# Performance work log

Measured on AMD Instinct MI355X. Metric: run time of the kernel, lower is better.

Reference implementation:

```python
import jax, jax.numpy as jnp
import numpy as np

EMBED_DIM = 768
NUM_HEADS = 12
HEAD_DIM = EMBED_DIM // NUM_HEADS
SCALE = HEAD_DIM ** -0.5


def setup_inputs() -> dict:
    key = jax.random.key(0)
    k_x, k_qkv, k_pw, k_pb = jax.random.split(key, 4)
    B, N, C = 8, 1024, EMBED_DIM
    x = jax.random.normal(k_x, (B, N, C), dtype=jnp.float32)
    # nn.Linear(embed_dim, 3*embed_dim, bias=False): weight [3C, C]
    w_qkv = jax.random.normal(k_qkv, (3 * C, C), dtype=jnp.float32) * (C ** -0.5)
    # nn.Linear(embed_dim, embed_dim): weight [C, C], bias [C]
    w_proj = jax.random.normal(k_pw, (C, C), dtype=jnp.float32) * (C ** -0.5)
    b_proj = jax.random.normal(k_pb, (C,), dtype=jnp.float32) * 0.01
    return {"x": x, "w_qkv": w_qkv, "w_proj": w_proj, "b_proj": b_proj}


def reference(x, w_qkv, w_proj, b_proj):
    B, N, C = x.shape
    H, D = NUM_HEADS, HEAD_DIM
    # qkv projection: [B, N, 3C] -> [3, B, H, N, D]
    qkv = jnp.einsum('bnc,ec->bne', x, w_qkv)
    qkv = qkv.reshape(B, N, 3, H, D).transpose(2, 0, 3, 1, 4)
    q, k, v = qkv[0], qkv[1], qkv[2]
    # explicit attention matrix [B, H, N, N]
    attn = jax.nn.softmax(jnp.einsum('bhnd,bhmd->bhnm', q, k) * SCALE, axis=-1)
    # attn @ v -> [B, N, C]
    out = jnp.einsum('bhnm,bhmd->bhnd', attn, v)
    out = out.transpose(0, 2, 1, 3).reshape(B, N, C)
    out = jnp.einsum('bnc,oc->bno', out, w_proj) + b_proj
    return out, attn
```

## Files before the change

kernel.cpp:

```cpp
#include <hip/hip_runtime.h>

#define B_ 8
#define N_ 1024
#define C_ 768
#define H_ 12
#define D_ 64
#define SCALE_ 0.125f

typedef _Float16 v8h __attribute__((ext_vector_type(8)));
typedef float v4f __attribute__((ext_vector_type(4)));

__device__ __forceinline__ void gload_lds16(const void* g, void* l) {
    __builtin_amdgcn_global_load_lds((const __attribute__((address_space(1))) void*)g,
                                     (__attribute__((address_space(3))) void*)l, 16, 0, 0);
}

__global__ __launch_bounds__(256) void cast_f2h(const float* __restrict__ src,
                                                _Float16* __restrict__ dst, int n8) {
    const int i = blockIdx.x * 256 + threadIdx.x;
    if (i < n8) {
        const v4f a = *(const v4f*)&src[(size_t)i * 8];
        const v4f b = *(const v4f*)&src[(size_t)i * 8 + 4];
        v8h o;
        o[0] = (_Float16)a[0]; o[1] = (_Float16)a[1]; o[2] = (_Float16)a[2]; o[3] = (_Float16)a[3];
        o[4] = (_Float16)b[0]; o[5] = (_Float16)b[1]; o[6] = (_Float16)b[2]; o[7] = (_Float16)b[3];
        *(v8h*)&dst[(size_t)i * 8] = o;
    }
}

__global__ __launch_bounds__(256) void gemm_qkv(const _Float16* __restrict__ X,
                                                const _Float16* __restrict__ W,
                                                _Float16* __restrict__ qh,
                                                _Float16* __restrict__ kh,
                                                _Float16* __restrict__ vth) {
    __shared__ _Float16 As[128 * 32];
    __shared__ _Float16 Bs[128 * 32];
    const int t = threadIdx.x;
    const int w = t >> 6, l = t & 63;
    const int q4 = l >> 4, c0 = l & 15;
    const int wm = w & 1, wn = w >> 1;
    const int m0 = blockIdx.x * 128, n0 = blockIdx.y * 128;
    const int sc8 = (t & 3) * 8;
    v4f acc[4][4] = {};
    for (int k0 = 0; k0 < C_; k0 += 32) {
        #pragma unroll
        for (int i = 0; i < 2; ++i) {
            const int row = i * 64 + (t >> 2);
            gload_lds16(&X[(size_t)(m0 + row) * C_ + k0 + sc8], &As[(i * 256 + t) * 8]);
            gload_lds16(&W[(size_t)(n0 + row) * C_ + k0 + sc8], &Bs[(i * 256 + t) * 8]);
        }
        __syncthreads();
        v8h a[4], b[4];
        #pragma unroll
        for (int mi = 0; mi < 4; ++mi)
            a[mi] = *(const v8h*)&As[(wm * 64 + mi * 16 + c0) * 32 + q4 * 8];
        #pragma unroll
        for (int ni = 0; ni < 4; ++ni)
            b[ni] = *(const v8h*)&Bs[(wn * 64 + ni * 16 + c0) * 32 + q4 * 8];
        #pragma unroll
        for (int mi = 0; mi < 4; ++mi)
            #pragma unroll
            for (int ni = 0; ni < 4; ++ni)
                acc[mi][ni] = __builtin_amdgcn_mfma_f32_16x16x32_f16(a[mi], b[ni], acc[mi][ni], 0, 0, 0);
        __syncthreads();
    }
    const int which = n0 / C_;
    const int nbase = n0 % C_;
    #pragma unroll
    for (int ni = 0; ni < 4; ++ni) {
        const int n = nbase + wn * 64 + ni * 16 + c0;
        const int h = n >> 6, d = n & 63;
        #pragma unroll
        for (int mi = 0; mi < 4; ++mi) {
            #pragma unroll
            for (int r = 0; r < 4; ++r) {
                const int m = m0 + wm * 64 + mi * 16 + q4 * 4 + r;
                const int b = m >> 10, nn = m & 1023;
                const _Float16 val = (_Float16)acc[mi][ni][r];
                if (which == 0)
                    qh[((size_t)(b * H_ + h) * N_ + nn) * D_ + d] = val;
                else if (which == 1)
                    kh[((size_t)(b * H_ + h) * N_ + nn) * D_ + d] = val;
                else
                    vth[((size_t)(b * H_ + h) * D_ + d) * N_ + nn] = val;
            }
        }
    }
}

__global__ __launch_bounds__(256) void attn_fused(const _Float16* __restrict__ qh,
                                                  const _Float16* __restrict__ kh,
                                                  const _Float16* __restrict__ vth,
                                                  float* __restrict__ attn,
                                                  _Float16* __restrict__ oah) {
    __shared__ _Float16 Qs[2 * 16 * 32];
    __shared__ _Float16 Ks[2 * 128 * 32];
    __shared__ _Float16 Vt[4 * 64 * 32];
    __shared__ float Ps[16 * 132];
    __shared__ float redm[64], reds[64];
    const int t = threadIdx.x;
    const int w = t >> 6, l = t & 63;
    const int q4 = l >> 4, c0 = l & 15;
    const int mt = blockIdx.x, bh = blockIdx.y;
    const size_t qkbase = (size_t)bh * N_ * D_;
    const size_t vtbase = (size_t)bh * D_ * N_;

    if (w < 2)
        gload_lds16(&qh[qkbase + (size_t)(mt * 16 + (l >> 2)) * D_ + w * 32 + (l & 3) * 8],
                    &Qs[t * 8]);
    #pragma unroll
    for (int i = 0; i < 4; ++i) {
        const int idx = i * 256 + t;
        const int p = idx >> 9, row = (idx & 511) >> 2, c8 = (idx & 3) * 8;
        gload_lds16(&kh[qkbase + (size_t)row * D_ + p * 32 + c8], &Ks[idx * 8]);
    }
    __syncthreads();
    v8h a0 = *(const v8h*)&Qs[c0 * 32 + q4 * 8];
    v8h a1 = *(const v8h*)&Qs[512 + c0 * 32 + q4 * 8];

    v4f S[16];
    #pragma unroll
    for (int i = 0; i < 16; ++i) S[i] = (v4f){0.f, 0.f, 0.f, 0.f};

    for (int c = 0; c < 8; ++c) {
        #pragma unroll
        for (int h2 = 0; h2 < 2; ++h2) {
            const int roff = (h2 * 64 + w * 16 + c0) * 32 + q4 * 8;
            const v8h b0 = *(const v8h*)&Ks[roff];
            const v8h b1 = *(const v8h*)&Ks[4096 + roff];
            v4f acc = __builtin_amdgcn_mfma_f32_16x16x32_f16(a0, b0, S[c * 2 + h2], 0, 0, 0);
            S[c * 2 + h2] = __builtin_amdgcn_mfma_f32_16x16x32_f16(a1, b1, acc, 0, 0, 0);
        }
        if (c < 7) {
            __syncthreads();
            #pragma unroll
            for (int i = 0; i < 4; ++i) {
                const int idx = i * 256 + t;
                const int p = idx >> 9, row = (idx & 511) >> 2, c8 = (idx & 3) * 8;
                gload_lds16(&kh[qkbase + (size_t)((c + 1) * 128 + row) * D_ + p * 32 + c8],
                            &Ks[idx * 8]);
            }
            __syncthreads();
        }
    }

    float mrow[4] = {-1e30f, -1e30f, -1e30f, -1e30f};
    #pragma unroll
    for (int kt = 0; kt < 16; ++kt)
        #pragma unroll
        for (int r = 0; r < 4; ++r) mrow[r] = fmaxf(mrow[r], S[kt][r]);
    #pragma unroll
    for (int r = 0; r < 4; ++r) {
        #pragma unroll
        for (int mask = 8; mask; mask >>= 1)
            mrow[r] = fmaxf(mrow[r], __shfl_xor(mrow[r], mask, 16));
    }
    if (c0 == 0) {
        #pragma unroll
        for (int r = 0; r < 4; ++r) redm[w * 16 + q4 * 4 + r] = mrow[r];
    }
    __syncthreads();
    #pragma unroll
    for (int r = 0; r < 4; ++r) {
        float mm = redm[q4 * 4 + r];
        mm = fmaxf(mm, redm[16 + q4 * 4 + r]);
        mm = fmaxf(mm, redm[32 + q4 * 4 + r]);
        mm = fmaxf(mm, redm[48 + q4 * 4 + r]);
        mrow[r] = mm;
    }
    float srow[4] = {0.f, 0.f, 0.f, 0.f};
    #pragma unroll
    for (int kt = 0; kt < 16; ++kt)
        #pragma unroll
        for (int r = 0; r < 4; ++r) {
            const float e = __expf((S[kt][r] - mrow[r]) * SCALE_);
            S[kt][r] = e;
            srow[r] += e;
        }
    #pragma unroll
    for (int r = 0; r < 4; ++r) {
        #pragma unroll
        for (int mask = 8; mask; mask >>= 1) srow[r] += __shfl_xor(srow[r], mask, 16);
    }
    if (c0 == 0) {
        #pragma unroll
        for (int r = 0; r < 4; ++r) reds[w * 16 + q4 * 4 + r] = srow[r];
    }
    __syncthreads();
    float inv[4];
    #pragma unroll
    for (int r = 0; r < 4; ++r)
        inv[r] = 1.0f / (reds[q4 * 4 + r] + reds[16 + q4 * 4 + r] +
                         reds[32 + q4 * 4 + r] + reds[48 + q4 * 4 + r]);

    v4f O = {0.f, 0.f, 0.f, 0.f};
    for (int s = 0; s < 8; ++s) {
        #pragma unroll
        for (int kt2 = 0; kt2 < 2; ++kt2)
            #pragma unroll
            for (int r = 0; r < 4; ++r)
                Ps[(q4 * 4 + r) * 132 + kt2 * 64 + w * 16 + c0] = S[s * 2 + kt2][r] * inv[r];
        #pragma unroll
        for (int i = 0; i < 4; ++i)
            gload_lds16(&vth[vtbase + (size_t)(t >> 2) * N_ + s * 128 + i * 32 + (t & 3) * 8],
                        &Vt[(i * 256 + t) * 8]);
        __syncthreads();
        #pragma unroll
        for (int i = 0; i < 2; ++i) {
            const int cidx = i * 256 + t;
            const int row = cidx >> 5, col = (cidx & 31) * 4;
            *(v4f*)&attn[((size_t)bh * N_ + mt * 16 + row) * N_ + s * 128 + col] =
                *(const v4f*)&Ps[row * 132 + col];
        }
        #pragma unroll
        for (int kk = 0; kk < 4; ++kk) {
            const float* pp = &Ps[c0 * 132 + kk * 32 + q4 * 8];
            const v4f p0 = *(const v4f*)pp;
            const v4f p1 = *(const v4f*)(pp + 4);
            v8h af;
            af[0] = (_Float16)p0[0]; af[1] = (_Float16)p0[1];
            af[2] = (_Float16)p0[2]; af[3] = (_Float16)p0[3];
            af[4] = (_Float16)p1[0]; af[5] = (_Float16)p1[1];
            af[6] = (_Float16)p1[2]; af[7] = (_Float16)p1[3];
            const v8h bf = *(const v8h*)&Vt[kk * 2048 + (w * 16 + c0) * 32 + q4 * 8];
            O = __builtin_amdgcn_mfma_f32_16x16x32_f16(af, bf, O, 0, 0, 0);
        }
        __syncthreads();
    }
    const int b = bh / H_, h = bh % H_;
    #pragma unroll
    for (int r = 0; r < 4; ++r)
        oah[((size_t)b * N_ + mt * 16 + q4 * 4 + r) * C_ + h * D_ + w * 16 + c0] = (_Float16)O[r];
}

__global__ __launch_bounds__(256) void gemm_proj(const _Float16* __restrict__ X,
                                                 const _Float16* __restrict__ W,
                                                 const float* __restrict__ Bias,
                                                 float* __restrict__ out) {
    __shared__ _Float16 As[128 * 32];
    __shared__ _Float16 Bs[128 * 32];
    const int t = threadIdx.x;
    const int w = t >> 6, l = t & 63;
    const int q4 = l >> 4, c0 = l & 15;
    const int wm = w & 1, wn = w >> 1;
    const int m0 = blockIdx.x * 128, n0 = blockIdx.y * 128;
    const int sc8 = (t & 3) * 8;
    v4f acc[4][4] = {};
    for (int k0 = 0; k0 < C_; k0 += 32) {
        #pragma unroll
        for (int i = 0; i < 2; ++i) {
            const int row = i * 64 + (t >> 2);
            gload_lds16(&X[(size_t)(m0 + row) * C_ + k0 + sc8], &As[(i * 256 + t) * 8]);
            gload_lds16(&W[(size_t)(n0 + row) * C_ + k0 + sc8], &Bs[(i * 256 + t) * 8]);
        }
        __syncthreads();
        v8h a[4], b[4];
        #pragma unroll
        for (int mi = 0; mi < 4; ++mi)
            a[mi] = *(const v8h*)&As[(wm * 64 + mi * 16 + c0) * 32 + q4 * 8];
        #pragma unroll
        for (int ni = 0; ni < 4; ++ni)
            b[ni] = *(const v8h*)&Bs[(wn * 64 + ni * 16 + c0) * 32 + q4 * 8];
        #pragma unroll
        for (int mi = 0; mi < 4; ++mi)
            #pragma unroll
            for (int ni = 0; ni < 4; ++ni)
                acc[mi][ni] = __builtin_amdgcn_mfma_f32_16x16x32_f16(a[mi], b[ni], acc[mi][ni], 0, 0, 0);
        __syncthreads();
    }
    #pragma unroll
    for (int ni = 0; ni < 4; ++ni) {
        const int n = n0 + wn * 64 + ni * 16 + c0;
        const float bias = Bias[n];
        #pragma unroll
        for (int mi = 0; mi < 4; ++mi) {
            #pragma unroll
            for (int r = 0; r < 4; ++r) {
                const int m = m0 + wm * 64 + mi * 16 + q4 * 4 + r;
                out[(size_t)m * C_ + n] = acc[mi][ni][r] + bias;
            }
        }
    }
}

extern "C" void kernel_launch(void* const* d_in, const int* in_sizes, int n_in,
                              void* d_out, int out_size, void* d_ws, size_t ws_size,
                              hipStream_t stream) {
    const float* x      = (const float*)d_in[0];
    const float* w_qkv  = (const float*)d_in[1];
    const float* w_proj = (const float*)d_in[2];
    const float* b_proj = (const float*)d_in[3];

    float* out  = (float*)d_out;
    float* attn = out + (size_t)B_ * N_ * C_;

    const size_t NX  = (size_t)B_ * N_ * C_;
    const size_t NWQ = (size_t)3 * C_ * C_;
    const size_t NWP = (size_t)C_ * C_;
    _Float16* xh  = (_Float16*)d_ws;
    _Float16* wqh = xh + NX;
    _Float16* wph = wqh + NWQ;
    _Float16* qh  = wph + NWP;
    _Float16* kh  = qh + NX;
    _Float16* vth = kh + NX;
    _Float16* oah = vth + NX;

    cast_f2h<<<dim3((int)(NX / 8 / 256)), 256, 0, stream>>>(x, xh, (int)(NX / 8));
    cast_f2h<<<dim3((int)(NWQ / 8 / 256)), 256, 0, stream>>>(w_qkv, wqh, (int)(NWQ / 8));
    cast_f2h<<<dim3((int)(NWP / 8 / 256)), 256, 0, stream>>>(w_proj, wph, (int)(NWP / 8));

    gemm_qkv  <<<dim3(64, 18), 256, 0, stream>>>(xh, wqh, qh, kh, vth);
    attn_fused<<<dim3(64, 96), 256, 0, stream>>>(qh, kh, vth, attn, oah);
    gemm_proj <<<dim3(64, 6), 256, 0, stream>>>(oah, wph, b_proj, out);
}
```

Measured before the change: 675.2 us.

## Double-buffer GEMM and attention tiles, widen attention blocks to 32 query rows

Both GEMMs now double-buffer their LDS tiles so the next K-slice loads while MFMAs run on the current one, and drop one barrier per iteration. The attention kernel is restructured to 512 threads covering 32 query rows, with double-buffered K, P and V^T tiles in 64-column chunks. The attention-matrix and output writes use nontemporal stores. This aims to hide global-load latency and reduce write-back traffic, at the cost of more LDS per block and a more complex sync schedule that could lower occupancy.

After: 577.9 us. 14.4% less time.

```diff
diff --git a/kernel.cpp b/kernel.cpp
--- a/kernel.cpp
+++ b/kernel.cpp
@@ -33,30 +33,43 @@
                                                 _Float16* __restrict__ qh,
                                                 _Float16* __restrict__ kh,
                                                 _Float16* __restrict__ vth) {
-    __shared__ _Float16 As[128 * 32];
-    __shared__ _Float16 Bs[128 * 32];
+    __shared__ _Float16 As[2 * 128 * 32];
+    __shared__ _Float16 Bs[2 * 128 * 32];
     const int t = threadIdx.x;
     const int w = t >> 6, l = t & 63;
     const int q4 = l >> 4, c0 = l & 15;
     const int wm = w & 1, wn = w >> 1;
     const int m0 = blockIdx.x * 128, n0 = blockIdx.y * 128;
     const int sc8 = (t & 3) * 8;
+    const int srow = t >> 2;
     v4f acc[4][4] = {};
-    for (int k0 = 0; k0 < C_; k0 += 32) {
-        #pragma unroll
-        for (int i = 0; i < 2; ++i) {
-            const int row = i * 64 + (t >> 2);
-            gload_lds16(&X[(size_t)(m0 + row) * C_ + k0 + sc8], &As[(i * 256 + t) * 8]);
-            gload_lds16(&W[(size_t)(n0 + row) * C_ + k0 + sc8], &Bs[(i * 256 + t) * 8]);
-        }
-        __syncthreads();
+    #pragma unroll
+    for (int i = 0; i < 2; ++i) {
+        const int row = i * 64 + srow;
+        gload_lds16(&X[(size_t)(m0 + row) * C_ + sc8], &As[(i * 256 + t) * 8]);
+        gload_lds16(&W[(size_t)(n0 + row) * C_ + sc8], &Bs[(i * 256 + t) * 8]);
+    }
+    __syncthreads();
+    int cb = 0;
+    for (int k0 = 0; k0 < C_; k0 += 32, cb ^= 1) {
+        if (k0 + 32 < C_) {
+            const int nb = cb ^ 1;
+            #pragma unroll
+            for (int i = 0; i < 2; ++i) {
+                const int row = i * 64 + srow;
+                gload_lds16(&X[(size_t)(m0 + row) * C_ + k0 + 32 + sc8],
+                            &As[(nb * 512 + i * 256 + t) * 8]);
+                gload_lds16(&W[(size_t)(n0 + row) * C_ + k0 + 32 + sc8],
+                            &Bs[(nb * 512 + i * 256 + t) * 8]);
+            }
+        }
         v8h a[4], b[4];
         #pragma unroll
         for (int mi = 0; mi < 4; ++mi)
-            a[mi] = *(const v8h*)&As[(wm * 64 + mi * 16 + c0) * 32 + q4 * 8];
+            a[mi] = *(const v8h*)&As[cb * 4096 + (wm * 64 + mi * 16 + c0) * 32 + q4 * 8];
         #pragma unroll
         for (int ni = 0; ni < 4; ++ni)
-            b[ni] = *(const v8h*)&Bs[(wn * 64 + ni * 16 + c0) * 32 + q4 * 8];
+            b[ni] = *(const v8h*)&Bs[cb * 4096 + (wn * 64 + ni * 16 + c0) * 32 + q4 * 8];
         #pragma unroll
         for (int mi = 0; mi < 4; ++mi)
             #pragma unroll
@@ -88,60 +101,53 @@
     }
 }
 
-__global__ __launch_bounds__(256) void attn_fused(const _Float16* __restrict__ qh,
-                                                  const _Float16* __restrict__ kh,
-                                                  const _Float16* __restrict__ vth,
-                                                  float* __restrict__ attn,
-                                                  _Float16* __restrict__ oah) {
-    __shared__ _Float16 Qs[2 * 16 * 32];
-    __shared__ _Float16 Ks[2 * 128 * 32];
-    __shared__ _Float16 Vt[4 * 64 * 32];
-    __shared__ float Ps[16 * 132];
-    __shared__ float redm[64], reds[64];
+__global__ __launch_bounds__(512, 4) void attn_fused(const _Float16* __restrict__ qh,
+                                                     const _Float16* __restrict__ kh,
+                                                     const _Float16* __restrict__ vth,
+                                                     float* __restrict__ attn,
+                                                     _Float16* __restrict__ oah) {
+    __shared__ _Float16 Qs[2 * 32 * 32];
+    __shared__ _Float16 Ks[2 * 2 * 64 * 32];
+    __shared__ _Float16 Vt[2 * 2 * 64 * 32];
+    __shared__ float Ps[2 * 32 * 68];
+    __shared__ float redm[128], reds[128];
     const int t = threadIdx.x;
     const int w = t >> 6, l = t & 63;
     const int q4 = l >> 4, c0 = l & 15;
+    const int wg = w >> 2, wl = w & 3;
     const int mt = blockIdx.x, bh = blockIdx.y;
     const size_t qkbase = (size_t)bh * N_ * D_;
     const size_t vtbase = (size_t)bh * D_ * N_;
-
-    if (w < 2)
-        gload_lds16(&qh[qkbase + (size_t)(mt * 16 + (l >> 2)) * D_ + w * 32 + (l & 3) * 8],
-                    &Qs[t * 8]);
-    #pragma unroll
-    for (int i = 0; i < 4; ++i) {
-        const int idx = i * 256 + t;
-        const int p = idx >> 9, row = (idx & 511) >> 2, c8 = (idx & 3) * 8;
-        gload_lds16(&kh[qkbase + (size_t)row * D_ + p * 32 + c8], &Ks[idx * 8]);
-    }
-    __syncthreads();
-    v8h a0 = *(const v8h*)&Qs[c0 * 32 + q4 * 8];
-    v8h a1 = *(const v8h*)&Qs[512 + c0 * 32 + q4 * 8];
+    const int sp  = t >> 8;
+    const int srw = (t >> 2) & 63;
+    const int sc8 = (t & 3) * 8;
+
+    if (t < 256) {
+        const int qp = t >> 7, qr = (t >> 2) & 31;
+        gload_lds16(&qh[qkbase + (size_t)(mt * 32 + qr) * D_ + qp * 32 + sc8], &Qs[t * 8]);
+    }
+    gload_lds16(&kh[qkbase + (size_t)srw * D_ + sp * 32 + sc8], &Ks[t * 8]);
+    __syncthreads();
+
+    const v8h a0 = *(const v8h*)&Qs[(wg * 16 + c0) * 32 + q4 * 8];
+    const v8h a1 = *(const v8h*)&Qs[1024 + (wg * 16 + c0) * 32 + q4 * 8];
 
     v4f S[16];
     #pragma unroll
     for (int i = 0; i < 16; ++i) S[i] = (v4f){0.f, 0.f, 0.f, 0.f};
 
-    for (int c = 0; c < 8; ++c) {
-        #pragma unroll
-        for (int h2 = 0; h2 < 2; ++h2) {
-            const int roff = (h2 * 64 + w * 16 + c0) * 32 + q4 * 8;
-            const v8h b0 = *(const v8h*)&Ks[roff];
-            const v8h b1 = *(const v8h*)&Ks[4096 + roff];
-            v4f acc = __builtin_amdgcn_mfma_f32_16x16x32_f16(a0, b0, S[c * 2 + h2], 0, 0, 0);
-            S[c * 2 + h2] = __builtin_amdgcn_mfma_f32_16x16x32_f16(a1, b1, acc, 0, 0, 0);
-        }
-        if (c < 7) {
-            __syncthreads();
-            #pragma unroll
-            for (int i = 0; i < 4; ++i) {
-                const int idx = i * 256 + t;
-                const int p = idx >> 9, row = (idx & 511) >> 2, c8 = (idx & 3) * 8;
-                gload_lds16(&kh[qkbase + (size_t)((c + 1) * 128 + row) * D_ + p * 32 + c8],
-                            &Ks[idx * 8]);
-            }
-            __syncthreads();
-        }
+    #pragma unroll
+    for (int c = 0; c < 16; ++c) {
+        const int kb = c & 1;
+        if (c < 15)
+            gload_lds16(&kh[qkbase + (size_t)((c + 1) * 64 + srw) * D_ + sp * 32 + sc8],
+                        &Ks[(kb ^ 1) * 4096 + t * 8]);
+        const int roff = (wl * 16 + c0) * 32 + q4 * 8;
+        const v8h b0 = *(const v8h*)&Ks[kb * 4096 + roff];
+        const v8h b1 = *(const v8h*)&Ks[kb * 4096 + 2048 + roff];
+        S[c] = __builtin_amdgcn_mfma_f32_16x16x32_f16(a0, b0, S[c], 0, 0, 0);
+        S[c] = __builtin_amdgcn_mfma_f32_16x16x32_f16(a1, b1, S[c], 0, 0, 0);
+        if (c < 15) __syncthreads();
     }
 
     float mrow[4] = {-1e30f, -1e30f, -1e30f, -1e30f};
@@ -160,13 +166,12 @@
         for (int r = 0; r < 4; ++r) redm[w * 16 + q4 * 4 + r] = mrow[r];
     }
     __syncthreads();
+    gload_lds16(&vth[vtbase + (size_t)srw * N_ + sp * 32 + sc8], &Vt[t * 8]);
     #pragma unroll
     for (int r = 0; r < 4; ++r) {
-        float mm = redm[q4 * 4 + r];
-        mm = fmaxf(mm, redm[16 + q4 * 4 + r]);
-        mm = fmaxf(mm, redm[32 + q4 * 4 + r]);
-        mm = fmaxf(mm, redm[48 + q4 * 4 + r]);
-        mrow[r] = mm;
+        const int base = wg * 64 + q4 * 4 + r;
+        mrow[r] = fmaxf(fmaxf(redm[base], redm[base + 16]),
+                        fmaxf(redm[base + 32], redm[base + 48]));
     }
     float srow[4] = {0.f, 0.f, 0.f, 0.f};
     #pragma unroll
@@ -189,32 +194,36 @@
     __syncthreads();
     float inv[4];
     #pragma unroll
+    for (int r = 0; r < 4; ++r) {
+        const int base = wg * 64 + q4 * 4 + r;
+        inv[r] = 1.0f / (reds[base] + reds[base + 16] + reds[base + 32] + reds[base + 48]);
+    }
+    #pragma unroll
     for (int r = 0; r < 4; ++r)
-        inv[r] = 1.0f / (reds[q4 * 4 + r] + reds[16 + q4 * 4 + r] +
-                         reds[32 + q4 * 4 + r] + reds[48 + q4 * 4 + r]);
+        Ps[(wg * 16 + q4 * 4 + r) * 68 + wl * 16 + c0] = S[0][r] * inv[r];
+    __syncthreads();
 
     v4f O = {0.f, 0.f, 0.f, 0.f};
-    for (int s = 0; s < 8; ++s) {
-        #pragma unroll
-        for (int kt2 = 0; kt2 < 2; ++kt2)
+    const int arow = t >> 4, acol = (t & 15) * 4;
+    float* attn_base = &attn[((size_t)bh * N_ + mt * 32 + arow) * N_ + acol];
+    #pragma unroll
+    for (int s = 0; s < 16; ++s) {
+        const int pb = s & 1;
+        if (s < 15) {
+            const int nb = pb ^ 1;
             #pragma unroll
             for (int r = 0; r < 4; ++r)
-                Ps[(q4 * 4 + r) * 132 + kt2 * 64 + w * 16 + c0] = S[s * 2 + kt2][r] * inv[r];
-        #pragma unroll
-        for (int i = 0; i < 4; ++i)
-            gload_lds16(&vth[vtbase + (size_t)(t >> 2) * N_ + s * 128 + i * 32 + (t & 3) * 8],
-                        &Vt[(i * 256 + t) * 8]);
-        __syncthreads();
-        #pragma unroll
-        for (int i = 0; i < 2; ++i) {
-            const int cidx = i * 256 + t;
-            const int row = cidx >> 5, col = (cidx & 31) * 4;
-            *(v4f*)&attn[((size_t)bh * N_ + mt * 16 + row) * N_ + s * 128 + col] =
-                *(const v4f*)&Ps[row * 132 + col];
-        }
-        #pragma unroll
-        for (int kk = 0; kk < 4; ++kk) {
-            const float* pp = &Ps[c0 * 132 + kk * 32 + q4 * 8];
+                Ps[nb * 2176 + (wg * 16 + q4 * 4 + r) * 68 + wl * 16 + c0] = S[s + 1][r] * inv[r];
+            gload_lds16(&vth[vtbase + (size_t)srw * N_ + (s + 1) * 64 + sp * 32 + sc8],
+                        &Vt[nb * 4096 + t * 8]);
+        }
+        {
+            const v4f pv = *(const v4f*)&Ps[pb * 2176 + arow * 68 + acol];
+            __builtin_nontemporal_store(pv, (v4f*)(attn_base + s * 64));
+        }
+        #pragma unroll
+        for (int kk = 0; kk < 2; ++kk) {
+            const float* pp = &Ps[pb * 2176 + (wg * 16 + c0) * 68 + kk * 32 + q4 * 8];
             const v4f p0 = *(const v4f*)pp;
             const v4f p1 = *(const v4f*)(pp + 4);
             v8h af;
@@ -222,45 +231,59 @@
             af[2] = (_Float16)p0[2]; af[3] = (_Float16)p0[3];
             af[4] = (_Float16)p1[0]; af[5] = (_Float16)p1[1];
             af[6] = (_Float16)p1[2]; af[7] = (_Float16)p1[3];
-            const v8h bf = *(const v8h*)&Vt[kk * 2048 + (w * 16 + c0) * 32 + q4 * 8];
+            const v8h bf = *(const v8h*)&Vt[pb * 4096 + kk * 2048 + (wl * 16 + c0) * 32 + q4 * 8];
             O = __builtin_amdgcn_mfma_f32_16x16x32_f16(af, bf, O, 0, 0, 0);
         }
-        __syncthreads();
+        if (s < 15) __syncthreads();
     }
     const int b = bh / H_, h = bh % H_;
     #pragma unroll
     for (int r = 0; r < 4; ++r)
-        oah[((size_t)b * N_ + mt * 16 + q4 * 4 + r) * C_ + h * D_ + w * 16 + c0] = (_Float16)O[r];
+        oah[((size_t)b * N_ + mt * 32 + wg * 16 + q4 * 4 + r) * C_ + h * D_ + wl * 16 + c0] =
+            (_Float16)O[r];
 }
 
 __global__ __launch_bounds__(256) void gemm_proj(const _Float16* __restrict__ X,
                                                  const _Float16* __restrict__ W,
                                                  const float* __restrict__ Bias,
                                                  float* __restrict__ out) {
-    __shared__ _Float16 As[128 * 32];
-    __shared__ _Float16 Bs[128 * 32];
+    __shared__ _Float16 As[2 * 128 * 32];
+    __shared__ _Float16 Bs[2 * 128 * 32];
     const int t = threadIdx.x;
     const int w = t >> 6, l = t & 63;
     const int q4 = l >> 4, c0 = l & 15;
     const int wm = w & 1, wn = w >> 1;
     const int m0 = blockIdx.x * 128, n0 = blockIdx.y * 128;
     const int sc8 = (t & 3) * 8;
+    const int srow = t >> 2;
     v4f acc[4][4] = {};
-    for (int k0 = 0; k0 < C_; k0 += 32) {
-        #pragma unroll
-        for (int i = 0; i < 2; ++i) {
-            const int row = i * 64 + (t >> 2);
-            gload_lds16(&X[(size_t)(m0 + row) * C_ + k0 + sc8], &As[(i * 256 + t) * 8]);
-            gload_lds16(&W[(size_t)(n0 + row) * C_ + k0 + sc8], &Bs[(i * 256 + t) * 8]);
-        }
-        __syncthreads();
+    #pragma unroll
+    for (int i = 0; i < 2; ++i) {
+        const int row = i * 64 + srow;
+        gload_lds16(&X[(size_t)(m0 + row) * C_ + sc8], &As[(i * 256 + t) * 8]);
+        gload_lds16(&W[(size_t)(n0 + row) * C_ + sc8], &Bs[(i * 256 + t) * 8]);
+    }
+    __syncthreads();
+    int cb = 0;
+    for (int k0 = 0; k0 < C_; k0 += 32, cb ^= 1) {
+        if (k0 + 32 < C_) {
+            const int nb = cb ^ 1;
+            #pragma unroll
+            for (int i = 0; i < 2; ++i) {
+                const int row = i * 64 + srow;
+                gload_lds16(&X[(size_t)(m0 + row) * C_ + k0 + 32 + sc8],
+                            &As[(nb * 512 + i * 256 + t) * 8]);
+                gload_lds16(&W[(size_t)(n0 + row) * C_ + k0 + 32 + sc8],
+                            &Bs[(nb * 512 + i * 256 + t) * 8]);
+            }
+        }
         v8h a[4], b[4];
         #pragma unroll
         for (int mi = 0; mi < 4; ++mi)
-            a[mi] = *(const v8h*)&As[(wm * 64 + mi * 16 + c0) * 32 + q4 * 8];
+            a[mi] = *(const v8h*)&As[cb * 4096 + (wm * 64 + mi * 16 + c0) * 32 + q4 * 8];
         #pragma unroll
         for (int ni = 0; ni < 4; ++ni)
-            b[ni] = *(const v8h*)&Bs[(wn * 64 + ni * 16 + c0) * 32 + q4 * 8];
+            b[ni] = *(const v8h*)&Bs[cb * 4096 + (wn * 64 + ni * 16 + c0) * 32 + q4 * 8];
         #pragma unroll
         for (int mi = 0; mi < 4; ++mi)
             #pragma unroll
@@ -277,7 +300,7 @@
             #pragma unroll
             for (int r = 0; r < 4; ++r) {
                 const int m = m0 + wm * 64 + mi * 16 + q4 * 4 + r;
-                out[(size_t)m * C_ + n] = acc[mi][ni][r] + bias;
+                __builtin_nontemporal_store(acc[mi][ni][r] + bias, &out[(size_t)m * C_ + n]);
             }
         }
     }
@@ -310,6 +333,6 @@
     cast_f2h<<<dim3((int)(NWP / 8 / 256)), 256, 0, stream>>>(w_proj, wph, (int)(NWP / 8));
 
     gemm_qkv  <<<dim3(64, 18), 256, 0, stream>>>(xh, wqh, qh, kh, vth);
-    attn_fused<<<dim3(64, 96), 256, 0, stream>>>(qh, kh, vth, attn, oah);
+    attn_fused<<<dim3(32, 96), 512, 0, stream>>>(qh, kh, vth, attn, oah);
     gemm_proj <<<dim3(64, 6), 256, 0, stream>>>(oah, wph, b_proj, out);
 }
```
